# Optimization experiments

Hardware: AMD Instinct MI355X
Metric: run time of the kernel (lower is better)

Reference implementation:

```python
import jax, jax.numpy as jnp
import numpy as np

B, D, N, S = 1024, 512, 500000, 32768


def setup_inputs() -> dict:
    key = jax.random.key(0)
    k1, k2, k3 = jax.random.split(key, 3)
    inputs = jax.random.normal(k1, (B, D), dtype=jnp.float32)
    # Linear(D, N) init: uniform(-0.05, 0.05) weight, zero bias
    weight = jax.random.uniform(k2, (N, D), dtype=jnp.float32, minval=-0.05, maxval=0.05)
    bias = jnp.zeros((N,), dtype=jnp.float32)
    sample_ids = jax.random.randint(k3, (S,), 0, N, dtype=jnp.int64)
    return {"inputs": inputs, "weight": weight, "bias": bias, "sample_ids": sample_ids}


def reference(inputs, weight, bias, sample_ids):
    # Gather retrieved class embeddings: [S, D] and their biases [S]
    sample_weights = weight[sample_ids]
    sample_bias = bias[sample_ids]
    # Sampled logits: inputs @ sample_weights.T + bias  -> [B, S]
    # (matches sample_weights.matmul(inputs.t()).t() + sample_bias in torch)
    logits = jnp.einsum("bd,sd->bs", inputs, sample_weights) + sample_bias
    return logits
```

## Files before the change

### kernel.cpp

```cpp
#include <hip/hip_runtime.h>
#include <stdint.h>

#define B_DIM 1024
#define D_DIM 512
#define S_DIM 32768

typedef __attribute__((ext_vector_type(8))) short bf16x8;
typedef __attribute__((ext_vector_type(4))) float f32x4;
typedef __attribute__((ext_vector_type(8))) unsigned short u16x8;

#define AS1 __attribute__((address_space(1)))
#define AS3 __attribute__((address_space(3)))

__device__ __forceinline__ unsigned short f2bf(float f) {
  union { float f; uint32_t u; } x; x.f = f;
  uint32_t r = x.u + 0x7fffu + ((x.u >> 16) & 1u);
  return (unsigned short)(r >> 16);
}
__device__ __forceinline__ uint32_t cvtpk(float a, float b) {
  uint32_t r;
  asm("v_cvt_pk_bf16_f32 %0, %1, %2" : "=v"(r) : "v"(a), "v"(b));
  return r;
}

__global__ __launch_bounds__(256) void conv_a(const float* __restrict__ A,
                                              unsigned short* __restrict__ Ab) {
  int gid = blockIdx.x * 256 + threadIdx.x;
  const float* src = A + (size_t)gid * 8;
  float4 v0 = *(const float4*)src;
  float4 v1 = *(const float4*)(src + 4);
  u16x8 o;
  o[0] = f2bf(v0.x); o[1] = f2bf(v0.y); o[2] = f2bf(v0.z); o[3] = f2bf(v0.w);
  o[4] = f2bf(v1.x); o[5] = f2bf(v1.y); o[6] = f2bf(v1.z); o[7] = f2bf(v1.w);
  *(u16x8*)(Ab + (size_t)gid * 8) = o;
}

#define BN 128
#define NG 64
#define B_OFF 32768

__global__ __launch_bounds__(512, 2) void gemm_fused(const unsigned short* __restrict__ Ab,
                                                     const float* __restrict__ W,
                                                     const float* __restrict__ bias,
                                                     const int* __restrict__ ids,
                                                     float* __restrict__ out) {
  __shared__ __attribute__((aligned(16))) char lds[163840];

  const int tid = threadIdx.x;
  const int lane = tid & 63;
  const int w = tid >> 6;
  const int wr = w >> 2;
  const int wc = w & 3;
  const int lq = lane >> 4;
  const int l16 = lane & 15;
  const int n0 = blockIdx.x * BN;

  {
    const int row = tid >> 2;
    const int c = tid & 3;
    const int myid = ids[n0 + row];
    const float* srcW = W + (size_t)myid * D_DIM;
    char* drow = lds + B_OFF + row * 1024;
    const int r7 = row & 7;
#pragma unroll
    for (int j = 0; j < 16; ++j) {
      const float* p = srcW + j * 32 + c * 8;
      float4 a = *(const float4*)p;
      float4 b = *(const float4*)(p + 4);
      int4 o;
      o.x = cvtpk(a.x, a.y); o.y = cvtpk(a.z, a.w);
      o.z = cvtpk(b.x, b.y); o.w = cvtpk(b.z, b.w);
      const int slot = (c + j * 4) ^ r7;
      *(int4*)(drow + slot * 16) = o;
    }
  }
  float bb[2];
#pragma unroll
  for (int n = 0; n < 2; ++n)
    bb[n] = bias[ids[n0 + wc * 32 + n * 16 + l16]];

  __syncthreads();

  const char* sA[2];
#pragma unroll
  for (int j = 0; j < 2; ++j) {
    const int P = j * 8192 + w * 1024 + lane * 16;
    const int L = P ^ (((P >> 7) & 7) << 4);
    sA[j] = (const char*)Ab + (size_t)(L >> 7) * 1024 + (L & 127);
  }
  auto stage = [&](int g) {
    const int off = ((g >> 3) << 17) + ((g & 7) << 7);
    char* bufa = lds + (g & 1) * 16384;
#pragma unroll
    for (int j = 0; j < 2; ++j)
      __builtin_amdgcn_global_load_lds((const AS1 void*)(sA[j] + off),
                                       (AS3 void*)(bufa + j * 8192 + w * 1024),
                                       16, 0, 0);
  };

  const int swz = (l16 & 7) << 4;
  int arow[4];
#pragma unroll
  for (int m = 0; m < 4; ++m) arow[m] = (wr * 64 + m * 16 + l16) * 128;
  int bbase[2], bx7[2];
#pragma unroll
  for (int n = 0; n < 2; ++n) {
    const int col = wc * 32 + n * 16 + l16;
    bbase[n] = B_OFF + col * 1024;
    bx7[n] = col & 7;
  }

  f32x4 acc[4][2];
#pragma unroll
  for (int m = 0; m < 4; ++m)
#pragma unroll
    for (int n = 0; n < 2; ++n)
      acc[m][n] = (f32x4)0.0f;

  stage(0);

  for (int g = 0; g < NG; ++g) {
    __builtin_amdgcn_sched_barrier(0);
    if (g < NG - 1) {
      stage(g + 1);
      __builtin_amdgcn_sched_barrier(0);
      asm volatile("s_waitcnt vmcnt(2)" ::: "memory");
    } else {
      asm volatile("s_waitcnt vmcnt(0)" ::: "memory");
    }
    __builtin_amdgcn_s_barrier();
    __builtin_amdgcn_sched_barrier(0);

    const char* bufa = lds + (g & 1) * 16384;
    const int ks = (g & 7) << 3;

#pragma unroll
    for (int kk = 0; kk < 2; ++kk) {
      bf16x8 af[4], bv[2];
#pragma unroll
      for (int m = 0; m < 4; ++m)
        af[m] = *(const bf16x8*)(bufa + ((arow[m] + kk * 64 + lq * 16) ^ swz));
#pragma unroll
      for (int n = 0; n < 2; ++n)
        bv[n] = *(const bf16x8*)(lds + bbase[n] +
                                 (((ks + kk * 4 + lq) ^ bx7[n]) << 4));
      __builtin_amdgcn_s_setprio(1);
#pragma unroll
      for (int m = 0; m < 4; ++m)
#pragma unroll
        for (int n = 0; n < 2; ++n)
          acc[m][n] = __builtin_amdgcn_mfma_f32_16x16x32_bf16(af[m], bv[n],
                                                              acc[m][n], 0, 0, 0);
      __builtin_amdgcn_s_setprio(0);
    }

    __builtin_amdgcn_sched_barrier(0);
    __builtin_amdgcn_s_barrier();

    if ((g & 7) == 7) {
      const int rt = (g >> 3) * 128 + wr * 64 + lq * 4;
#pragma unroll
      for (int n = 0; n < 2; ++n) {
        const int col = n0 + wc * 32 + n * 16 + l16;
#pragma unroll
        for (int m = 0; m < 4; ++m) {
          const int rbase = rt + m * 16;
#pragma unroll
          for (int r = 0; r < 4; ++r)
            out[(size_t)(rbase + r) * S_DIM + col] = acc[m][n][r] + bb[n];
          acc[m][n] = (f32x4)0.0f;
        }
      }
    }
  }
}

extern "C" void kernel_launch(void* const* d_in, const int* in_sizes, int n_in,
                              void* d_out, int out_size, void* d_ws, size_t ws_size,
                              hipStream_t stream) {
  const float* inp  = (const float*)d_in[0];
  const float* W    = (const float*)d_in[1];
  const float* bias = (const float*)d_in[2];
  const int*   ids  = (const int*)d_in[3];
  float* out = (float*)d_out;

  unsigned short* Ab = (unsigned short*)d_ws;

  conv_a<<<(B_DIM * D_DIM / 8) / 256, 256, 0, stream>>>(inp, Ab);

  dim3 grid(S_DIM / BN);
  gemm_fused<<<grid, 512, 0, stream>>>(Ab, W, bias, ids, out);
}
```

Baseline: 66.09 us.

## Use 256-row A tiles with 4x4 warp tiles and prefetch before W gather

Changes the A staging so each stage loads 256 rows by 32 k-elements (one MFMA k-step) instead of 128 rows by 64, with a new swizzled layout. Warps are rearranged 4x2 so each computes a 64x64 tile (4x4 MFMAs) rather than 64x32, which raises MFMA work per LDS fragment load and doubles the accumulators. The first A stage is issued before the W gather and conversion so it overlaps with that prologue. The per-stage barrier count is unchanged, but accumulator register pressure rises, which may hurt occupancy at 2 blocks per CU.

Result: slower. 68.07 us (+3.0%).

```diff
diff --git a/kernel.cpp b/kernel.cpp
--- a/kernel.cpp
+++ b/kernel.cpp
@@ -49,11 +49,31 @@
   const int tid = threadIdx.x;
   const int lane = tid & 63;
   const int w = tid >> 6;
-  const int wr = w >> 2;
-  const int wc = w & 3;
+  const int wm = w >> 1;
+  const int wn = w & 1;
   const int lq = lane >> 4;
   const int l16 = lane & 15;
   const int n0 = blockIdx.x * BN;
+
+  const char* srcA[2];
+#pragma unroll
+  for (int j = 0; j < 2; ++j) {
+    const int p = j * 512 + tid;
+    const int line = p >> 3;
+    const int sl = (p & 7) ^ (line & 7);
+    const int row = line * 2 + (sl >> 2);
+    srcA[j] = (const char*)Ab + row * 1024 + (sl & 3) * 16;
+  }
+  auto stage = [&](int g) {
+    const int off = (g >> 4) * 262144 + (g & 15) * 64;
+    char* dst = lds + (g & 1) * 16384 + w * 1024;
+#pragma unroll
+    for (int j = 0; j < 2; ++j)
+      __builtin_amdgcn_global_load_lds((const AS1 void*)(srcA[j] + off),
+                                       (AS3 void*)(dst + j * 8192), 16, 0, 0);
+  };
+
+  stage(0);
 
   {
     const int row = tid >> 2;
@@ -74,50 +94,34 @@
       *(int4*)(drow + slot * 16) = o;
     }
   }
-  float bb[2];
+  float bb[4];
 #pragma unroll
-  for (int n = 0; n < 2; ++n)
-    bb[n] = bias[ids[n0 + wc * 32 + n * 16 + l16]];
+  for (int n = 0; n < 4; ++n)
+    bb[n] = bias[ids[n0 + wn * 64 + n * 16 + l16]];
 
   __syncthreads();
 
-  const char* sA[2];
+  int aoff[4];
 #pragma unroll
-  for (int j = 0; j < 2; ++j) {
-    const int P = j * 8192 + w * 1024 + lane * 16;
-    const int L = P ^ (((P >> 7) & 7) << 4);
-    sA[j] = (const char*)Ab + (size_t)(L >> 7) * 1024 + (L & 127);
+  for (int m = 0; m < 4; ++m) {
+    const int row = wm * 64 + m * 16 + l16;
+    const int s = (((row & 1) << 2) | lq) ^ ((row >> 1) & 7);
+    aoff[m] = (row >> 1) * 128 + s * 16;
   }
-  auto stage = [&](int g) {
-    const int off = ((g >> 3) << 17) + ((g & 7) << 7);
-    char* bufa = lds + (g & 1) * 16384;
+  int bbase[4], bx7[4];
 #pragma unroll
-    for (int j = 0; j < 2; ++j)
-      __builtin_amdgcn_global_load_lds((const AS1 void*)(sA[j] + off),
-                                       (AS3 void*)(bufa + j * 8192 + w * 1024),
-                                       16, 0, 0);
-  };
-
-  const int swz = (l16 & 7) << 4;
-  int arow[4];
-#pragma unroll
-  for (int m = 0; m < 4; ++m) arow[m] = (wr * 64 + m * 16 + l16) * 128;
-  int bbase[2], bx7[2];
-#pragma unroll
-  for (int n = 0; n < 2; ++n) {
-    const int col = wc * 32 + n * 16 + l16;
+  for (int n = 0; n < 4; ++n) {
+    const int col = wn * 64 + n * 16 + l16;
     bbase[n] = B_OFF + col * 1024;
     bx7[n] = col & 7;
   }
 
-  f32x4 acc[4][2];
+  f32x4 acc[4][4];
 #pragma unroll
   for (int m = 0; m < 4; ++m)
 #pragma unroll
-    for (int n = 0; n < 2; ++n)
+    for (int n = 0; n < 4; ++n)
       acc[m][n] = (f32x4)0.0f;
-
-  stage(0);
 
   for (int g = 0; g < NG; ++g) {
     __builtin_amdgcn_sched_barrier(0);
@@ -132,36 +136,33 @@
     __builtin_amdgcn_sched_barrier(0);
 
     const char* bufa = lds + (g & 1) * 16384;
-    const int ks = (g & 7) << 3;
+    const int kt4 = (g & 15) << 2;
 
+    bf16x8 af[4], bv[4];
 #pragma unroll
-    for (int kk = 0; kk < 2; ++kk) {
-      bf16x8 af[4], bv[2];
+    for (int m = 0; m < 4; ++m)
+      af[m] = *(const bf16x8*)(bufa + aoff[m]);
 #pragma unroll
-      for (int m = 0; m < 4; ++m)
-        af[m] = *(const bf16x8*)(bufa + ((arow[m] + kk * 64 + lq * 16) ^ swz));
+    for (int n = 0; n < 4; ++n)
+      bv[n] = *(const bf16x8*)(lds + bbase[n] + (((kt4 + lq) ^ bx7[n]) << 4));
+
+    __builtin_amdgcn_s_setprio(1);
 #pragma unroll
-      for (int n = 0; n < 2; ++n)
-        bv[n] = *(const bf16x8*)(lds + bbase[n] +
-                                 (((ks + kk * 4 + lq) ^ bx7[n]) << 4));
-      __builtin_amdgcn_s_setprio(1);
+    for (int m = 0; m < 4; ++m)
 #pragma unroll
-      for (int m = 0; m < 4; ++m)
-#pragma unroll
-        for (int n = 0; n < 2; ++n)
-          acc[m][n] = __builtin_amdgcn_mfma_f32_16x16x32_bf16(af[m], bv[n],
-                                                              acc[m][n], 0, 0, 0);
-      __builtin_amdgcn_s_setprio(0);
-    }
+      for (int n = 0; n < 4; ++n)
+        acc[m][n] = __builtin_amdgcn_mfma_f32_16x16x32_bf16(af[m], bv[n],
+                                                            acc[m][n], 0, 0, 0);
+    __builtin_amdgcn_s_setprio(0);
 
     __builtin_amdgcn_sched_barrier(0);
     __builtin_amdgcn_s_barrier();
 
-    if ((g & 7) == 7) {
-      const int rt = (g >> 3) * 128 + wr * 64 + lq * 4;
+    if ((g & 15) == 15) {
+      const int rt = (g >> 4) * 256 + wm * 64 + lq * 4;
 #pragma unroll
-      for (int n = 0; n < 2; ++n) {
-        const int col = n0 + wc * 32 + n * 16 + l16;
+      for (int n = 0; n < 4; ++n) {
+        const int col = n0 + wn * 64 + n * 16 + l16;
 #pragma unroll
         for (int m = 0; m < 4; ++m) {
           const int rbase = rt + m * 16;
```
